# Performance work log

Hardware: AMD Instinct MI355X
Metric: run time of the kernel (lower is better)

## Reference

```python
import jax, jax.numpy as jnp
import numpy as np

STRIDE = 16      # image -> feature stride (224 -> 14)
POOL = 7         # ROI pool output grid
FG_HI = 0.85
FG_LO = 0.5


def setup_inputs() -> dict:
    key = jax.random.key(0)
    ks = jax.random.split(key, 8)
    B, N, M, K = 4, 128, 16, 80
    Cf, Tf, Cs, Ts, H, W = 256, 32, 2048, 8, 14, 14
    fast = jax.random.normal(ks[0], (B, Cf, Tf, H, W), jnp.float32)
    slow = jax.random.normal(ks[1], (B, Cs, Ts, H, W), jnp.float32)
    # valid gt boxes inside 224x224
    xy = jax.random.uniform(ks[2], (B, M, 2)) * 160.0
    wh = 32.0 + jax.random.uniform(ks[3], (B, M, 2)) * 48.0
    gt = jnp.concatenate([xy, xy + wh], axis=-1)
    # proposals: first M coincide with gt (guarantees IoU>=0.85 foreground), rest random
    pxy = jax.random.uniform(ks[4], (B, N - M, 2)) * 160.0
    pwh = 16.0 + jax.random.uniform(ks[5], (B, N - M, 2)) * 64.0
    props = jnp.concatenate([gt, jnp.concatenate([pxy, pxy + pwh], axis=-1)], axis=1)
    gt_classes = (jax.random.uniform(ks[6], (B, M, K)) < 0.1).astype(jnp.float32)
    C = Cf + Cs
    W_cls = jax.random.normal(ks[7], (C, K), jnp.float32) * 0.02
    b_cls = jnp.zeros((K,), jnp.float32)
    return dict(fast_feature=fast, slow_feature=slow, proposal_bboxes=props,
                gt_bboxes_batch=gt, gt_classes_batch=gt_classes,
                W_cls=W_cls, b_cls=b_cls)


def _iou(a, b):
    # a: [B,N,4], b: [B,M,4] (x1,y1,x2,y2) -> [B,N,M]
    tl = jnp.maximum(a[:, :, None, :2], b[:, None, :, :2])
    br = jnp.minimum(a[:, :, None, 2:], b[:, None, :, 2:])
    inter = jnp.prod(jnp.clip(br - tl, 0.0), axis=-1)
    area_a = jnp.prod(a[:, :, 2:] - a[:, :, :2], axis=-1)[:, :, None]
    area_b = jnp.prod(b[:, :, 2:] - b[:, :, :2], axis=-1)[:, None, :]
    return inter / (area_a + area_b - inter)


def _roi_pool(feat, boxes):
    # feat: [B,C,H,W]; boxes: [B,N,4] in image coords -> [B,N,P,P,C]
    B, C, H, W = feat.shape
    fb = boxes / STRIDE
    x1, y1, x2, y2 = fb[..., 0], fb[..., 1], fb[..., 2], fb[..., 3]
    grid = (jnp.arange(POOL, dtype=feat.dtype) + 0.5) / POOL          # [P]
    cy = y1[..., None] + grid * (y2 - y1)[..., None]                  # [B,N,P]
    cx = x1[..., None] + grid * (x2 - x1)[..., None]                  # [B,N,P]
    iy = jnp.clip(jnp.floor(cy), 0, H - 1).astype(jnp.int32)
    ix = jnp.clip(jnp.floor(cx), 0, W - 1).astype(jnp.int32)
    ft = jnp.transpose(feat, (0, 2, 3, 1))                            # [B,H,W,C]
    bidx = jnp.arange(B)[:, None, None, None]
    return ft[bidx, iy[:, :, :, None], ix[:, :, None, :]]             # [B,N,P,P,C]


def reference(fast_feature, slow_feature, proposal_bboxes, gt_bboxes_batch,
              gt_classes_batch, W_cls, b_cls):
    # temporal average pooling (AvgPool3d over full T) + channel concat, fast first
    fast = fast_feature.mean(axis=2)
    slow = slow_feature.mean(axis=2)
    feature = jnp.concatenate([fast, slow], axis=1)                   # [B,C,H,W]

    # IoU-based foreground assignment
    ious = _iou(proposal_bboxes, gt_bboxes_batch)                     # [B,N,M]
    max_ious = ious.max(axis=2)                                       # [B,N]
    assign = ious.argmax(axis=2)                                      # [B,N]
    fg_hi = max_ious >= FG_HI
    fg = jnp.where(fg_hi.any(), fg_hi, max_ious >= FG_LO)             # global fallback
    labels = jnp.take_along_axis(gt_classes_batch, assign[:, :, None], axis=1)  # [B,N,K]

    # ROI pooling (dense over all proposals; non-fg are masked out of the loss)
    pool = _roi_pool(feature, proposal_bboxes)                        # [B,N,P,P,C]
    hid = pool.mean(axis=(2, 3))                                      # [B,N,C]
    logits = jnp.einsum('bnc,ck->bnk', hid, W_cls) + b_cls            # [B,N,K]

    # multilabel soft margin loss per proposal (mean over classes)
    per = -(labels * jax.nn.log_sigmoid(logits)
            + (1.0 - labels) * jax.nn.log_sigmoid(-logits)).mean(axis=-1)  # [B,N]
    fgf = fg.astype(per.dtype)
    cnt = fgf.sum(axis=1)
    cross_entropies = jnp.where(cnt > 0, (per * fgf).sum(axis=1) / jnp.maximum(cnt, 1.0), 0.0)
    return cross_entropies  # [B]
```

## Files before the change

### kernel.cpp

```cpp
#include <hip/hip_runtime.h>
#include <math.h>

#define BB 4
#define NN 128
#define MM 16
#define KK 80
#define CF 256
#define CSL 2048
#define CT 2304
#define TFAST 32
#define TSLOW 8
#define HH 14
#define WW 14
#define HWQ 196
#define NQ4 49

#define FEAT_OFF   0
#define FEAT_SIZE  (BB*CT*HWQ)
#define G_OFF      (FEAT_OFF + FEAT_SIZE)
#define G_SIZE     (BB*HWQ*KK)
#define FGF_OFF    (G_OFF + G_SIZE)
#define ASSIGN_OFF (FGF_OFF + BB*NN)
#define NUM_OFF    (ASSIGN_OFF + BB*NN)
#define CNT_OFF    (NUM_OFF + BB)
#define P_OFF      (CNT_OFF + BB)

#define NSPLIT 32
#define CCH    (CT/NSPLIT)
#define P_SIZE (NSPLIT*G_SIZE)

__global__ __launch_bounds__(256) void k1_tmean(const float* __restrict__ fast,
                                                const float* __restrict__ slow,
                                                float* __restrict__ ws) {
    int idx = blockIdx.x * blockDim.x + threadIdx.x;
    if (idx < G_SIZE) ws[G_OFF + idx] = 0.f;
    const int total = BB * CT * NQ4;
    if (idx >= total) return;
    int q  = idx % NQ4;
    int bc = idx / NQ4;
    int c  = bc % CT;
    int b  = bc / CT;
    float4 acc = make_float4(0.f, 0.f, 0.f, 0.f);
    if (c < CF) {
        const float4* p = (const float4*)(fast + (size_t)(b*CF + c) * TFAST * HWQ) + q;
        #pragma unroll 8
        for (int t = 0; t < TFAST; ++t) {
            float4 v = p[t * (HWQ/4)];
            acc.x += v.x; acc.y += v.y; acc.z += v.z; acc.w += v.w;
        }
        const float s = 1.f / TFAST;
        acc.x *= s; acc.y *= s; acc.z *= s; acc.w *= s;
    } else {
        const float4* p = (const float4*)(slow + (size_t)(b*CSL + (c-CF)) * TSLOW * HWQ) + q;
        #pragma unroll
        for (int t = 0; t < TSLOW; ++t) {
            float4 v = p[t * (HWQ/4)];
            acc.x += v.x; acc.y += v.y; acc.z += v.z; acc.w += v.w;
        }
        const float s = 1.f / TSLOW;
        acc.x *= s; acc.y *= s; acc.z *= s; acc.w *= s;
    }
    ((float4*)(ws + FEAT_OFF))[bc * NQ4 + q] = acc;
}

__global__ __launch_bounds__(256) void k2_gemm(const float* __restrict__ Wc,
                                               float* __restrict__ ws,
                                               int use_partials) {
    __shared__ float sfeat[CCH*HWQ];
    __shared__ float sW[CCH*KK];
    int bid = blockIdx.x;
    int b  = bid >> 6;
    int r  = bid & 63;
    int kh = r >> 5;
    int cs = r & 31;
    int c0 = cs * CCH;
    int tid = threadIdx.x;

    const float4* fsrc = (const float4*)(ws + FEAT_OFF + (size_t)(b*CT + c0) * HWQ);
    float4* fdst = (float4*)sfeat;
    #pragma unroll
    for (int i = 0; i < 14; ++i) {
        int x = tid + i*256;
        if (x < CCH*HWQ/4) fdst[x] = fsrc[x];
    }
    const float4* wsrc = (const float4*)(Wc + c0*KK);
    float4* wdst = (float4*)sW;
    #pragma unroll
    for (int i = 0; i < 6; ++i) {
        int x = tid + i*256;
        if (x < CCH*KK/4) wdst[x] = wsrc[x];
    }
    __syncthreads();

    int kq = tid & 7;
    int cg = tid >> 3;
    float acc[7][5];
    #pragma unroll
    for (int j = 0; j < 7; ++j)
        #pragma unroll
        for (int i = 0; i < 5; ++i) acc[j][i] = 0.f;

    const float* fr = sfeat + cg;
    const float* wr = sW + kh*40 + kq*5;
    #pragma unroll 2
    for (int c = 0; c < CCH; ++c) {
        float w0 = wr[c*KK+0], w1 = wr[c*KK+1], w2 = wr[c*KK+2],
              w3 = wr[c*KK+3], w4 = wr[c*KK+4];
        #pragma unroll
        for (int j = 0; j < 7; ++j) {
            float fv = fr[c*HWQ + 32*j];
            acc[j][0] += fv*w0; acc[j][1] += fv*w1; acc[j][2] += fv*w2;
            acc[j][3] += fv*w3; acc[j][4] += fv*w4;
        }
    }

    int k0 = kh*40 + kq*5;
    if (use_partials) {
        float* P = ws + P_OFF + (size_t)cs*G_SIZE + (size_t)b*HWQ*KK;
        #pragma unroll
        for (int j = 0; j < 7; ++j) {
            int cell = cg + 32*j;
            if (cell < HWQ) {
                #pragma unroll
                for (int i = 0; i < 5; ++i) P[cell*KK + k0 + i] = acc[j][i];
            }
        }
    } else {
        float* g = ws + G_OFF + (size_t)b*HWQ*KK;
        #pragma unroll
        for (int j = 0; j < 7; ++j) {
            int cell = cg + 32*j;
            if (cell < HWQ) {
                #pragma unroll
                for (int i = 0; i < 5; ++i) atomicAdd(&g[cell*KK + k0 + i], acc[j][i]);
            }
        }
    }
}

__global__ __launch_bounds__(256) void k2b_reduce(float* __restrict__ ws) {
    int idx = blockIdx.x * 256 + threadIdx.x;
    if (idx >= G_SIZE) return;
    const float* P = ws + P_OFF;
    float s = 0.f;
    #pragma unroll
    for (int cs = 0; cs < NSPLIT; ++cs) s += P[(size_t)cs*G_SIZE + idx];
    ws[G_OFF + idx] = s;
}

__global__ __launch_bounds__(512) void k3a_assign(const float* __restrict__ props,
                                                  const float* __restrict__ gtb,
                                                  float* __restrict__ ws) {
    __shared__ float sgt[BB*MM*4];
    __shared__ float sfg[BB*NN];
    __shared__ int sany;
    int t = threadIdx.x;
    if (t < BB*MM*4) sgt[t] = gtb[t];
    if (t == 0) sany = 0;
    __syncthreads();
    int b = t >> 7;
    float x1 = props[t*4+0], y1 = props[t*4+1], x2 = props[t*4+2], y2 = props[t*4+3];
    float aa = (x2 - x1) * (y2 - y1);
    float best = -1.f; int arg = 0;
    for (int m = 0; m < MM; ++m) {
        const float* g = &sgt[(b*MM + m)*4];
        float tlx = fmaxf(x1, g[0]), tly = fmaxf(y1, g[1]);
        float brx = fminf(x2, g[2]), bry = fminf(y2, g[3]);
        float inter = fmaxf(brx - tlx, 0.f) * fmaxf(bry - tly, 0.f);
        float ab = (g[2] - g[0]) * (g[3] - g[1]);
        float iou = inter / (aa + ab - inter);
        if (iou > best) { best = iou; arg = m; }
    }
    if (best >= 0.85f) atomicOr(&sany, 1);
    __syncthreads();
    float fg = sany ? (best >= 0.85f ? 1.f : 0.f) : (best >= 0.5f ? 1.f : 0.f);
    sfg[t] = fg;
    ws[FGF_OFF + t] = fg;
    ((int*)ws)[ASSIGN_OFF + t] = arg;
    __syncthreads();
    if (t < BB) {
        float s = 0.f;
        for (int i = 0; i < NN; ++i) s += sfg[t*NN + i];
        ws[CNT_OFF + t] = s;
        ws[NUM_OFF + t] = 0.f;
    }
}

__device__ __forceinline__ float logsig(float x) {
    return fminf(x, 0.f) - log1pf(expf(-fabsf(x)));
}

__global__ __launch_bounds__(128) void k3b_loss(const float* __restrict__ props,
                                                const float* __restrict__ gtc,
                                                const float* __restrict__ bcls,
                                                float* __restrict__ ws) {
    int p = blockIdx.x;
    int b = p >> 7;
    if (ws[FGF_OFF + p] == 0.f) return;
    __shared__ int cells[49];
    __shared__ float red[128];
    int t = threadIdx.x;
    if (t < 49) {
        int gy = t / 7, gx = t % 7;
        float x1 = props[p*4+0] * (1.f/16.f);
        float y1 = props[p*4+1] * (1.f/16.f);
        float x2 = props[p*4+2] * (1.f/16.f);
        float y2 = props[p*4+3] * (1.f/16.f);
        float gry = ((float)gy + 0.5f) / 7.f;
        float grx = ((float)gx + 0.5f) / 7.f;
        float cy = y1 + gry * (y2 - y1);
        float cx = x1 + grx * (x2 - x1);
        int iy = (int)floorf(cy); iy = min(max(iy, 0), HH-1);
        int ix = (int)floorf(cx); ix = min(max(ix, 0), WW-1);
        cells[t] = iy * WW + ix;
    }
    __syncthreads();
    float lk = 0.f;
    if (t < KK) {
        float acc = 0.f;
        const float* Gb = ws + G_OFF + b * HWQ * KK + t;
        #pragma unroll 7
        for (int g = 0; g < 49; ++g) acc += Gb[cells[g] * KK];
        float logit = acc * (1.f/49.f) + bcls[t];
        int a = ((const int*)ws)[ASSIGN_OFF + p];
        float y = gtc[(b*MM + a)*KK + t];
        lk = -(y * logsig(logit) + (1.f - y) * logsig(-logit));
    }
    red[t] = lk;
    __syncthreads();
    for (int s = 64; s > 0; s >>= 1) {
        if (t < s) red[t] += red[t + s];
        __syncthreads();
    }
    if (t == 0) atomicAdd(&ws[NUM_OFF + b], red[0] * (1.f/KK));
}

__global__ __launch_bounds__(64) void k3c_final(const float* __restrict__ ws,
                                                float* __restrict__ out) {
    int t = threadIdx.x;
    if (t < BB) {
        float c = ws[CNT_OFF + t];
        out[t] = (c > 0.f) ? ws[NUM_OFF + t] / c : 0.f;
    }
}

extern "C" void kernel_launch(void* const* d_in, const int* in_sizes, int n_in,
                              void* d_out, int out_size, void* d_ws, size_t ws_size,
                              hipStream_t stream) {
    const float* fast  = (const float*)d_in[0];
    const float* slow  = (const float*)d_in[1];
    const float* props = (const float*)d_in[2];
    const float* gtb   = (const float*)d_in[3];
    const float* gtc   = (const float*)d_in[4];
    const float* Wc    = (const float*)d_in[5];
    const float* bcls  = (const float*)d_in[6];
    float* ws  = (float*)d_ws;
    float* out = (float*)d_out;

    const size_t need = (size_t)(P_OFF + P_SIZE) * sizeof(float);
    const int use_partials = (ws_size >= need) ? 1 : 0;

    const int k1_threads = BB * CT * NQ4;
    k1_tmean<<<(k1_threads + 255)/256, 256, 0, stream>>>(fast, slow, ws);
    k2_gemm<<<BB * 2 * NSPLIT, 256, 0, stream>>>(Wc, ws, use_partials);
    if (use_partials)
        k2b_reduce<<<(G_SIZE + 255)/256, 256, 0, stream>>>(ws);
    k3a_assign<<<1, 512, 0, stream>>>(props, gtb, ws);
    k3b_loss<<<BB*NN, 128, 0, stream>>>(props, gtc, bcls, ws);
    k3c_final<<<1, 64, 0, stream>>>(ws, out);
}
```

Baseline: 140.0 us.

## Merge reduce with assignment and fold final kernel into loss via last-block counter

```diff
diff --git a/kernel.cpp b/kernel.cpp
--- a/kernel.cpp
+++ b/kernel.cpp
@@ -23,7 +23,8 @@
 #define ASSIGN_OFF (FGF_OFF + BB*NN)
 #define NUM_OFF    (ASSIGN_OFF + BB*NN)
 #define CNT_OFF    (NUM_OFF + BB)
-#define P_OFF      (CNT_OFF + BB)
+#define CTR_OFF    (CNT_OFF + BB)
+#define P_OFF      (CTR_OFF + 8)
 
 #define NSPLIT 32
 #define CCH    (CT/NSPLIT)
@@ -138,23 +139,28 @@
     }
 }
 
-__global__ __launch_bounds__(256) void k2b_reduce(float* __restrict__ ws) {
-    int idx = blockIdx.x * 256 + threadIdx.x;
-    if (idx >= G_SIZE) return;
-    const float* P = ws + P_OFF;
-    float s = 0.f;
-    #pragma unroll
-    for (int cs = 0; cs < NSPLIT; ++cs) s += P[(size_t)cs*G_SIZE + idx];
-    ws[G_OFF + idx] = s;
-}
-
-__global__ __launch_bounds__(512) void k3a_assign(const float* __restrict__ props,
+#define RED_BLOCKS ((G_SIZE + 511) / 512)
+__global__ __launch_bounds__(512) void k2b_assign(const float* __restrict__ props,
                                                   const float* __restrict__ gtb,
-                                                  float* __restrict__ ws) {
+                                                  float* __restrict__ ws,
+                                                  int use_partials) {
+    int blk = blockIdx.x;
+    int t = threadIdx.x;
+    if (blk < RED_BLOCKS) {
+        if (!use_partials) return;
+        int idx = blk * 512 + t;
+        if (idx < G_SIZE) {
+            const float* P = ws + P_OFF;
+            float s = 0.f;
+            #pragma unroll
+            for (int cs = 0; cs < NSPLIT; ++cs) s += P[(size_t)cs*G_SIZE + idx];
+            ws[G_OFF + idx] = s;
+        }
+        return;
+    }
     __shared__ float sgt[BB*MM*4];
     __shared__ float sfg[BB*NN];
     __shared__ int sany;
-    int t = threadIdx.x;
     if (t < BB*MM*4) sgt[t] = gtb[t];
     if (t == 0) sany = 0;
     __syncthreads();
@@ -184,6 +190,7 @@
         ws[CNT_OFF + t] = s;
         ws[NUM_OFF + t] = 0.f;
     }
+    if (t == 0) ((int*)ws)[CTR_OFF] = 0;
 }
 
 __device__ __forceinline__ float logsig(float x) {
@@ -193,54 +200,60 @@
 __global__ __launch_bounds__(128) void k3b_loss(const float* __restrict__ props,
                                                 const float* __restrict__ gtc,
                                                 const float* __restrict__ bcls,
-                                                float* __restrict__ ws) {
+                                                float* __restrict__ ws,
+                                                float* __restrict__ out) {
     int p = blockIdx.x;
     int b = p >> 7;
-    if (ws[FGF_OFF + p] == 0.f) return;
+    int t = threadIdx.x;
     __shared__ int cells[49];
     __shared__ float red[128];
-    int t = threadIdx.x;
-    if (t < 49) {
-        int gy = t / 7, gx = t % 7;
-        float x1 = props[p*4+0] * (1.f/16.f);
-        float y1 = props[p*4+1] * (1.f/16.f);
-        float x2 = props[p*4+2] * (1.f/16.f);
-        float y2 = props[p*4+3] * (1.f/16.f);
-        float gry = ((float)gy + 0.5f) / 7.f;
-        float grx = ((float)gx + 0.5f) / 7.f;
-        float cy = y1 + gry * (y2 - y1);
-        float cx = x1 + grx * (x2 - x1);
-        int iy = (int)floorf(cy); iy = min(max(iy, 0), HH-1);
-        int ix = (int)floorf(cx); ix = min(max(ix, 0), WW-1);
-        cells[t] = iy * WW + ix;
-    }
-    __syncthreads();
-    float lk = 0.f;
-    if (t < KK) {
-        float acc = 0.f;
-        const float* Gb = ws + G_OFF + b * HWQ * KK + t;
-        #pragma unroll 7
-        for (int g = 0; g < 49; ++g) acc += Gb[cells[g] * KK];
-        float logit = acc * (1.f/49.f) + bcls[t];
-        int a = ((const int*)ws)[ASSIGN_OFF + p];
-        float y = gtc[(b*MM + a)*KK + t];
-        lk = -(y * logsig(logit) + (1.f - y) * logsig(-logit));
-    }
-    red[t] = lk;
-    __syncthreads();
-    for (int s = 64; s > 0; s >>= 1) {
-        if (t < s) red[t] += red[t + s];
+    if (ws[FGF_OFF + p] != 0.f) {
+        if (t < 49) {
+            int gy = t / 7, gx = t % 7;
+            float x1 = props[p*4+0] * (1.f/16.f);
+            float y1 = props[p*4+1] * (1.f/16.f);
+            float x2 = props[p*4+2] * (1.f/16.f);
+            float y2 = props[p*4+3] * (1.f/16.f);
+            float gry = ((float)gy + 0.5f) / 7.f;
+            float grx = ((float)gx + 0.5f) / 7.f;
+            float cy = y1 + gry * (y2 - y1);
+            float cx = x1 + grx * (x2 - x1);
+            int iy = (int)floorf(cy); iy = min(max(iy, 0), HH-1);
+            int ix = (int)floorf(cx); ix = min(max(ix, 0), WW-1);
+            cells[t] = iy * WW + ix;
+        }
         __syncthreads();
-    }
-    if (t == 0) atomicAdd(&ws[NUM_OFF + b], red[0] * (1.f/KK));
-}
-
-__global__ __launch_bounds__(64) void k3c_final(const float* __restrict__ ws,
-                                                float* __restrict__ out) {
-    int t = threadIdx.x;
-    if (t < BB) {
-        float c = ws[CNT_OFF + t];
-        out[t] = (c > 0.f) ? ws[NUM_OFF + t] / c : 0.f;
+        float lk = 0.f;
+        if (t < KK) {
+            float acc = 0.f;
+            const float* Gb = ws + G_OFF + b * HWQ * KK + t;
+            #pragma unroll 7
+            for (int g = 0; g < 49; ++g) acc += Gb[cells[g] * KK];
+            float logit = acc * (1.f/49.f) + bcls[t];
+            int a = ((const int*)ws)[ASSIGN_OFF + p];
+            float y = gtc[(b*MM + a)*KK + t];
+            lk = -(y * logsig(logit) + (1.f - y) * logsig(-logit));
+        }
+        red[t] = lk;
+        __syncthreads();
+        for (int s = 64; s > 0; s >>= 1) {
+            if (t < s) red[t] += red[t + s];
+            __syncthreads();
+        }
+        if (t == 0) atomicAdd(&ws[NUM_OFF + b], red[0] * (1.f/KK));
+    }
+    if (t == 0) {
+        __threadfence();
+        int old = atomicAdd(&((int*)ws)[CTR_OFF], 1);
+        if (old == BB*NN - 1) {
+            __threadfence();
+            #pragma unroll
+            for (int bb = 0; bb < BB; ++bb) {
+                float num = atomicAdd(&ws[NUM_OFF + bb], 0.f);
+                float c = ws[CNT_OFF + bb];
+                out[bb] = (c > 0.f) ? num / c : 0.f;
+            }
+        }
     }
 }
 
@@ -263,9 +276,6 @@
     const int k1_threads = BB * CT * NQ4;
     k1_tmean<<<(k1_threads + 255)/256, 256, 0, stream>>>(fast, slow, ws);
     k2_gemm<<<BB * 2 * NSPLIT, 256, 0, stream>>>(Wc, ws, use_partials);
-    if (use_partials)
-        k2b_reduce<<<(G_SIZE + 255)/256, 256, 0, stream>>>(ws);
-    k3a_assign<<<1, 512, 0, stream>>>(props, gtb, ws);
-    k3b_loss<<<BB*NN, 128, 0, stream>>>(props, gtc, bcls, ws);
-    k3c_final<<<1, 64, 0, stream>>>(ws, out);
-}
+    k2b_assign<<<RED_BLOCKS + 1, 512, 0, stream>>>(props, gtb, ws, use_partials);
+    k3b_loss<<<BB*NN, 128, 0, stream>>>(props, gtc, bcls, ws, out);
+}
```

Result: slower. 143.4 us (+2.4%).
